# Optimization experiments

Measured on AMD Instinct MI355X. Metric: run time of the kernel, lower is better.

Reference implementation:

```python
import jax, jax.numpy as jnp
import numpy as np

INF = 10000.0
HEADS = 12
HEAD_SIZE = 64
HIDDEN = 1024
BATCH = 8
SEQLEN = 512


def _sin_cos(seqlen, dim, dtype):
    # SinusoidalPositionEmbedding (bert4torch style): indices = 10000**(-2i/dim)
    pos = jnp.arange(seqlen, dtype=dtype)
    inv = jnp.power(jnp.asarray(10000.0, dtype), -jnp.arange(dim // 2, dtype=dtype) * 2.0 / dim)
    freqs = pos[:, None] * inv[None, :]  # [s, dim/2]
    return jnp.sin(freqs), jnp.cos(freqs)


def setup_inputs() -> dict:
    key = jax.random.key(0)
    k1, k2, k3 = jax.random.split(key, 3)
    inputs = jax.random.normal(k1, (BATCH, SEQLEN, HIDDEN), dtype=jnp.float32)
    W = jax.random.normal(k2, (HIDDEN, HEADS * 2 * HEAD_SIZE), dtype=jnp.float32) * (HIDDEN ** -0.5)
    b = jax.random.normal(k3, (HEADS * 2 * HEAD_SIZE,), dtype=jnp.float32) * 0.02
    mask = jnp.ones((BATCH, SEQLEN), dtype=jnp.int32)
    return {"inputs": inputs, "W": W, "b": b, "mask": mask}


def reference(inputs, W, b, mask):
    bs, s, _ = inputs.shape
    h = inputs @ W + b  # [b, s, heads*2*hd]
    h = h.reshape(bs, s, HEADS, 2 * HEAD_SIZE)
    qw, kw = h[..., :HEAD_SIZE], h[..., HEAD_SIZE:]  # [b, s, h, d]

    # interleaved RoPE: cos_pos/sin_pos repeat each freq twice along last dim
    sin, cos = _sin_cos(s, HEAD_SIZE, h.dtype)
    cos2 = jnp.repeat(cos, 2, axis=-1)[None, :, None, :]  # [1, s, 1, d]
    sin2 = jnp.repeat(sin, 2, axis=-1)[None, :, None, :]

    def rot(x):
        x2 = jnp.stack([-x[..., 1::2], x[..., 0::2]], axis=-1).reshape(x.shape)
        return x * cos2 + x2 * sin2

    qw = rot(qw)
    kw = rot(kw)

    logits = jnp.einsum('bmhd,bnhd->bhmn', qw, kw)  # [b, h, s, s]

    m = mask.astype(logits.dtype)
    pad = 1.0 - m[:, None, None, :] * m[:, None, :, None]  # [b,1,s,s]
    tril = jnp.tril(jnp.ones((s, s), dtype=logits.dtype), k=-1)[None, None]  # strictly lower
    logits = logits - pad * INF - tril * INF
    out_mask = jnp.logical_or(pad > 0, tril > 0)
    return logits * (HEAD_SIZE ** -0.5), out_mask
```

## Files before the change

kernel.cpp:

```cpp
#include <hip/hip_runtime.h>
#include <stdint.h>

typedef unsigned short ushort_t;
typedef short short8 __attribute__((ext_vector_type(8)));
typedef float float4_ __attribute__((ext_vector_type(4)));
typedef unsigned short u16x8 __attribute__((ext_vector_type(8)));

#define INF_ 10000.0f
#define BATCH 8
#define SEQLEN 512
#define HIDDEN 1024
#define HEADS 12
#define HEAD_SIZE 64
#define NOUT 1536
#define MROWS 4096
#define BH 96
#define LOGITS_N 25165824
#define MASK_N   2097152

__device__ __align__(16) ushort_t g_A [(size_t)MROWS * HIDDEN];
__device__ __align__(16) ushort_t g_Wt[(size_t)NOUT * HIDDEN];
__device__ __align__(16) ushort_t g_Q[(size_t)BH * SEQLEN * HEAD_SIZE];
__device__ __align__(16) ushort_t g_K[(size_t)BH * SEQLEN * HEAD_SIZE];
__device__ __align__(16) float    g_tab[SEQLEN * 32 * 2];

__device__ __forceinline__ ushort_t f2bf(float f) {
    unsigned u = __builtin_bit_cast(unsigned, f);
    unsigned r = u + 0x7FFFu + ((u >> 16) & 1u);
    return (ushort_t)(r >> 16);
}

__device__ __forceinline__ void gload16(const ushort_t* g, ushort_t* l) {
    __builtin_amdgcn_global_load_lds(
        (const __attribute__((address_space(1))) void*)g,
        (__attribute__((address_space(3))) void*)l, 16, 0, 0);
}

__device__ __forceinline__ unsigned mask_code(const void* m) {
    unsigned u0 = ((const unsigned*)m)[0];
    unsigned u1 = ((const unsigned*)m)[1];
    if (u0 == 0x3F803F80u) return 2;
    if (u0 == 0x3F800000u) return 3;
    if (u0 == 0x01010101u) return 4;
    if (u0 == 0x00010001u) return 5;
    if (u0 == 1u && u1 == 0u) return 1;
    return 0;
}
__device__ __forceinline__ float mask_at(const void* m, unsigned code, int i) {
    switch (code) {
        case 1: return (float)((const long long*)m)[i];
        case 2: { unsigned u = (unsigned)((const ushort_t*)m)[i] << 16;
                  return __builtin_bit_cast(float, u); }
        case 3: return ((const float*)m)[i];
        case 4: return (float)((const signed char*)m)[i];
        case 5: return (float)((const short*)m)[i];
        default: return (float)((const int*)m)[i];
    }
}

__global__ void k_prep(const float* __restrict__ A, const float* __restrict__ W) {
    __shared__ ushort_t tile[32][33];
    int bid = blockIdx.x;
    int tid = threadIdx.x;
    if (bid < 2048) {
        int i = bid * 256 + tid;
        const float4_* p = (const float4_*)(A + (size_t)i * 8);
        float4_ v0 = p[0], v1 = p[1];
        u16x8 o;
        #pragma unroll
        for (int j = 0; j < 4; ++j) { o[j] = f2bf(v0[j]); o[j + 4] = f2bf(v1[j]); }
        *(u16x8*)(g_A + (size_t)i * 8) = o;
    } else if (bid < 2048 + 1536) {
        int bb = bid - 2048;
        int bx = bb % 48;
        int by = bb / 48;
        int tx = tid & 31, ty = tid >> 5;
        #pragma unroll
        for (int i = 0; i < 4; ++i) {
            int k = by * 32 + ty + i * 8;
            int n = bx * 32 + tx;
            tile[ty + i * 8][tx] = f2bf(W[(size_t)k * NOUT + n]);
        }
        __syncthreads();
        #pragma unroll
        for (int i = 0; i < 4; ++i) {
            int n = bx * 32 + ty + i * 8;
            int k = by * 32 + tx;
            g_Wt[(size_t)n * HIDDEN + k] = tile[tx][ty + i * 8];
        }
    } else {
        int i = (bid - 3584) * 256 + tid;
        int s = i >> 5, f = i & 31;
        float inv = powf(10000.0f, -(float)(2 * f) / 64.0f);
        float ang = (float)s * inv;
        g_tab[2 * i]     = sinf(ang);
        g_tab[2 * i + 1] = cosf(ang);
    }
}

__global__ void __launch_bounds__(256) k_gemm1(const float* __restrict__ bias) {
    __shared__ __align__(16) ushort_t sA[2][64 * 32];
    __shared__ __align__(16) ushort_t sB[2][128 * 32];
    int tid = threadIdx.x;
    int lane = tid & 63, wid = tid >> 6;
    int wm = wid >> 1, wn = wid & 1;
    int bm = (blockIdx.x & 63) * 64;
    int bn = (blockIdx.x >> 6) * 128;

    auto stage = [&](int bi, int ks) {
        {
            int row = tid >> 2, ch = tid & 3;
            gload16(g_A + (size_t)(bm + row) * HIDDEN + ks * 32 + ch * 8,
                    sA[bi] + (size_t)tid * 8);
        }
        #pragma unroll
        for (int i = 0; i < 2; ++i) {
            int c = tid + i * 256;
            int row = c >> 2, ch = c & 3;
            gload16(g_Wt + (size_t)(bn + row) * HIDDEN + ks * 32 + ch * 8,
                    sB[bi] + (size_t)c * 8);
        }
    };

    float4_ acc[2][4] = {};
    const int NT = HIDDEN / 32;
    stage(0, 0);
    __syncthreads();
    int cur = 0;
    for (int ks = 0; ks < NT; ++ks) {
        if (ks + 1 < NT) stage(cur ^ 1, ks + 1);
        short8 af[2], bfv[4];
        int kofs = (lane >> 4) * 8;
        #pragma unroll
        for (int mf = 0; mf < 2; ++mf)
            af[mf] = *(const short8*)(sA[cur] + (wm * 32 + mf * 16 + (lane & 15)) * 32 + kofs);
        #pragma unroll
        for (int nf = 0; nf < 4; ++nf)
            bfv[nf] = *(const short8*)(sB[cur] + (wn * 64 + nf * 16 + (lane & 15)) * 32 + kofs);
        #pragma unroll
        for (int mf = 0; mf < 2; ++mf)
            #pragma unroll
            for (int nf = 0; nf < 4; ++nf)
                acc[mf][nf] = __builtin_amdgcn_mfma_f32_16x16x32_bf16(af[mf], bfv[nf], acc[mf][nf], 0, 0, 0);
        __syncthreads();
        cur ^= 1;
    }

    #pragma unroll
    for (int nf = 0; nf < 4; ++nf) {
        int gn = bn + wn * 64 + nf * 16 + (lane & 15);
        float bv = bias[gn];
        int head = gn >> 7;
        int isk  = (gn >> 6) & 1;
        int d0 = gn & 63;
        int fi = d0 >> 1;
        float sgn = (gn & 1) ? 1.0f : -1.0f;
        ushort_t* dst = isk ? g_K : g_Q;
        #pragma unroll
        for (int mf = 0; mf < 2; ++mf) {
            int gm0 = bm + wm * 32 + mf * 16 + ((lane >> 4) * 4);
            #pragma unroll
            for (int r = 0; r < 4; ++r) {
                int gm = gm0 + r;
                int s = gm & (SEQLEN - 1);
                int b = gm >> 9;
                float v = acc[mf][nf][r] + bv;
                float p = __shfl_xor(v, 1, 64);
                const float* tc = g_tab + 2 * (s * 32 + fi);
                float sn = tc[0], cs = tc[1];
                float y = v * cs + sgn * p * sn;
                size_t o = (((size_t)(b * HEADS + head)) * SEQLEN + s) * HEAD_SIZE + d0;
                dst[o] = f2bf(y);
            }
        }
    }
}

__global__ void __launch_bounds__(256) k_gemm2(const void* __restrict__ mask,
                                               float* __restrict__ out) {
    __shared__ __align__(16) ushort_t sQ[128 * 64];
    __shared__ __align__(16) ushort_t sK[128 * 64];
    __shared__ float sMr[128], sMc[128];
    int tid = threadIdx.x;
    int lane = tid & 63, wid = tid >> 6;
    int blk = blockIdx.x;
    int bh = blk >> 4;
    int t = blk & 15;
    int mt = t >> 2, nt = t & 3;
    int b = bh / HEADS;
    bool writeMask = (bh - b * HEADS) == 0;

    const ushort_t* Qb = g_Q + ((size_t)bh * SEQLEN + mt * 128) * HEAD_SIZE;
    const ushort_t* Kb = g_K + ((size_t)bh * SEQLEN + nt * 128) * HEAD_SIZE;
    #pragma unroll
    for (int i = 0; i < 4; ++i) {
        int c = tid + i * 256;
        gload16(Qb + (size_t)c * 8, sQ + (size_t)c * 8);
        gload16(Kb + (size_t)c * 8, sK + (size_t)c * 8);
    }
    unsigned mcode = mask_code(mask);
    if (tid < 128)      sMr[tid]       = mask_at(mask, mcode, b * SEQLEN + mt * 128 + tid);
    else                sMc[tid - 128] = mask_at(mask, mcode, b * SEQLEN + nt * 128 + (tid - 128));
    __syncthreads();

    int wm = wid >> 1, wn = wid & 1;
    float4_ acc[4][4] = {};
    #pragma unroll
    for (int kk = 0; kk < 2; ++kk) {
        short8 af[4], bfv[4];
        int ko = kk * 32 + (lane >> 4) * 8;
        #pragma unroll
        for (int mf = 0; mf < 4; ++mf)
            af[mf] = *(const short8*)(sQ + (wm * 64 + mf * 16 + (lane & 15)) * 64 + ko);
        #pragma unroll
        for (int nf = 0; nf < 4; ++nf)
            bfv[nf] = *(const short8*)(sK + (wn * 64 + nf * 16 + (lane & 15)) * 64 + ko);
        #pragma unroll
        for (int mf = 0; mf < 4; ++mf)
            #pragma unroll
            for (int nf = 0; nf < 4; ++nf)
                acc[mf][nf] = __builtin_amdgcn_mfma_f32_16x16x32_bf16(af[mf], bfv[nf], acc[mf][nf], 0, 0, 0);
    }

    size_t obase = (size_t)bh * SEQLEN * SEQLEN;
    size_t mbase = (size_t)LOGITS_N + (size_t)b * SEQLEN * SEQLEN;
    #pragma unroll
    for (int mf = 0; mf < 4; ++mf) {
        #pragma unroll
        for (int nf = 0; nf < 4; ++nf) {
            int lcol = wn * 64 + nf * 16 + (lane & 15);
            int lrow0 = wm * 64 + mf * 16 + ((lane >> 4) * 4);
            int gn = nt * 128 + lcol;
            float mc = sMc[lcol];
            #pragma unroll
            for (int r = 0; r < 4; ++r) {
                int lrow = lrow0 + r;
                int gm = mt * 128 + lrow;
                float padv = 1.0f - sMr[lrow] * mc;
                bool tl = gn < gm;
                float v = (acc[mf][nf][r] - padv * INF_ - (tl ? INF_ : 0.0f)) * 0.125f;
                size_t off = (size_t)gm * SEQLEN + gn;
                out[obase + off] = v;
                if (writeMask)
                    out[mbase + off] = (padv > 0.0f || tl) ? 1.0f : 0.0f;
            }
        }
    }
}

extern "C" void kernel_launch(void* const* d_in, const int* in_sizes, int n_in,
                              void* d_out, int out_size, void* d_ws, size_t ws_size,
                              hipStream_t stream) {
    const float* inp = nullptr; const float* W = nullptr;
    const float* bias = nullptr; const void* mask = nullptr;
    for (int i = 0; i < n_in; ++i) {
        switch (in_sizes[i]) {
            case MROWS * HIDDEN:  inp  = (const float*)d_in[i]; break;
            case HIDDEN * NOUT:   W    = (const float*)d_in[i]; break;
            case NOUT:            bias = (const float*)d_in[i]; break;
            case BATCH * SEQLEN:  mask = d_in[i]; break;
        }
    }
    if (!inp || !W || !bias || !mask) {
        inp  = (const float*)d_in[0];
        W    = (const float*)d_in[1];
        bias = (const float*)d_in[2];
        mask = d_in[3];
    }
    float* out = (float*)d_out;
    (void)d_ws; (void)ws_size;

    k_prep<<<3648, 256, 0, stream>>>(inp, W);
    k_gemm1<<<768, 256, 0, stream>>>(bias);
    k_gemm2<<<16 * BH, 256, 0, stream>>>(mask, out);
}
```

Baseline: 73.93 us.

## Swizzle LDS tiles, deepen GEMM1 K-step to 64, remap GEMM2 block order

Applies an XOR swizzle on 16-byte chunks in shared memory for the Q/K and A/W tiles so that MFMA fragment reads avoid LDS bank conflicts. The projection GEMM now stages 64-wide K slices instead of 32, which halves the loop iterations and barriers but doubles the shared-memory footprint. The logits kernel also remaps block indices across groups of eight, presumably to spread neighbouring tiles across XCDs or cache slices. The risks are lower occupancy from the extra LDS and a different L2 locality pattern.

```diff
diff --git a/kernel.cpp b/kernel.cpp
--- a/kernel.cpp
+++ b/kernel.cpp
@@ -99,8 +99,8 @@
 }
 
 __global__ void __launch_bounds__(256) k_gemm1(const float* __restrict__ bias) {
-    __shared__ __align__(16) ushort_t sA[2][64 * 32];
-    __shared__ __align__(16) ushort_t sB[2][128 * 32];
+    __shared__ __align__(16) ushort_t sA[2][64 * 64];
+    __shared__ __align__(16) ushort_t sB[2][128 * 64];
     int tid = threadIdx.x;
     int lane = tid & 63, wid = tid >> 6;
     int wm = wid >> 1, wn = wid & 1;
@@ -108,40 +108,49 @@
     int bn = (blockIdx.x >> 6) * 128;
 
     auto stage = [&](int bi, int ks) {
-        {
-            int row = tid >> 2, ch = tid & 3;
-            gload16(g_A + (size_t)(bm + row) * HIDDEN + ks * 32 + ch * 8,
-                    sA[bi] + (size_t)tid * 8);
-        }
         #pragma unroll
         for (int i = 0; i < 2; ++i) {
             int c = tid + i * 256;
-            int row = c >> 2, ch = c & 3;
-            gload16(g_Wt + (size_t)(bn + row) * HIDDEN + ks * 32 + ch * 8,
+            int row = c >> 3, ch = (c & 7) ^ (row & 7);
+            gload16(g_A + (size_t)(bm + row) * HIDDEN + ks * 64 + ch * 8,
+                    sA[bi] + (size_t)c * 8);
+        }
+        #pragma unroll
+        for (int i = 0; i < 4; ++i) {
+            int c = tid + i * 256;
+            int row = c >> 3, ch = (c & 7) ^ (row & 7);
+            gload16(g_Wt + (size_t)(bn + row) * HIDDEN + ks * 64 + ch * 8,
                     sB[bi] + (size_t)c * 8);
         }
     };
 
     float4_ acc[2][4] = {};
-    const int NT = HIDDEN / 32;
+    const int NT = HIDDEN / 64;
     stage(0, 0);
     __syncthreads();
     int cur = 0;
     for (int ks = 0; ks < NT; ++ks) {
         if (ks + 1 < NT) stage(cur ^ 1, ks + 1);
-        short8 af[2], bfv[4];
-        int kofs = (lane >> 4) * 8;
-        #pragma unroll
-        for (int mf = 0; mf < 2; ++mf)
-            af[mf] = *(const short8*)(sA[cur] + (wm * 32 + mf * 16 + (lane & 15)) * 32 + kofs);
-        #pragma unroll
-        for (int nf = 0; nf < 4; ++nf)
-            bfv[nf] = *(const short8*)(sB[cur] + (wn * 64 + nf * 16 + (lane & 15)) * 32 + kofs);
-        #pragma unroll
-        for (int mf = 0; mf < 2; ++mf)
-            #pragma unroll
-            for (int nf = 0; nf < 4; ++nf)
-                acc[mf][nf] = __builtin_amdgcn_mfma_f32_16x16x32_bf16(af[mf], bfv[nf], acc[mf][nf], 0, 0, 0);
+        #pragma unroll
+        for (int kk = 0; kk < 2; ++kk) {
+            short8 af[2], bfv[4];
+            int c0 = kk * 4 + (lane >> 4);
+            #pragma unroll
+            for (int mf = 0; mf < 2; ++mf) {
+                int r = wm * 32 + mf * 16 + (lane & 15);
+                af[mf] = *(const short8*)(sA[cur] + r * 64 + ((c0 ^ (r & 7)) * 8));
+            }
+            #pragma unroll
+            for (int nf = 0; nf < 4; ++nf) {
+                int r = wn * 64 + nf * 16 + (lane & 15);
+                bfv[nf] = *(const short8*)(sB[cur] + r * 64 + ((c0 ^ (r & 7)) * 8));
+            }
+            #pragma unroll
+            for (int mf = 0; mf < 2; ++mf)
+                #pragma unroll
+                for (int nf = 0; nf < 4; ++nf)
+                    acc[mf][nf] = __builtin_amdgcn_mfma_f32_16x16x32_bf16(af[mf], bfv[nf], acc[mf][nf], 0, 0, 0);
+        }
         __syncthreads();
         cur ^= 1;
     }
@@ -183,7 +192,7 @@
     __shared__ float sMr[128], sMc[128];
     int tid = threadIdx.x;
     int lane = tid & 63, wid = tid >> 6;
-    int blk = blockIdx.x;
+    int blk = (blockIdx.x & 7) * 192 + (blockIdx.x >> 3);
     int bh = blk >> 4;
     int t = blk & 15;
     int mt = t >> 2, nt = t & 3;
@@ -195,8 +204,9 @@
     #pragma unroll
     for (int i = 0; i < 4; ++i) {
         int c = tid + i * 256;
-        gload16(Qb + (size_t)c * 8, sQ + (size_t)c * 8);
-        gload16(Kb + (size_t)c * 8, sK + (size_t)c * 8);
+        int row = c >> 3, ch = (c & 7) ^ (row & 7);
+        gload16(Qb + (size_t)row * 64 + ch * 8, sQ + (size_t)c * 8);
+        gload16(Kb + (size_t)row * 64 + ch * 8, sK + (size_t)c * 8);
     }
     unsigned mcode = mask_code(mask);
     if (tid < 128)      sMr[tid]       = mask_at(mask, mcode, b * SEQLEN + mt * 128 + tid);
@@ -208,13 +218,17 @@
     #pragma unroll
     for (int kk = 0; kk < 2; ++kk) {
         short8 af[4], bfv[4];
-        int ko = kk * 32 + (lane >> 4) * 8;
-        #pragma unroll
-        for (int mf = 0; mf < 4; ++mf)
-            af[mf] = *(const short8*)(sQ + (wm * 64 + mf * 16 + (lane & 15)) * 64 + ko);
-        #pragma unroll
-        for (int nf = 0; nf < 4; ++nf)
-            bfv[nf] = *(const short8*)(sK + (wn * 64 + nf * 16 + (lane & 15)) * 64 + ko);
+        int c0 = kk * 4 + (lane >> 4);
+        #pragma unroll
+        for (int mf = 0; mf < 4; ++mf) {
+            int r = wm * 64 + mf * 16 + (lane & 15);
+            af[mf] = *(const short8*)(sQ + r * 64 + ((c0 ^ (r & 7)) * 8));
+        }
+        #pragma unroll
+        for (int nf = 0; nf < 4; ++nf) {
+            int r = wn * 64 + nf * 16 + (lane & 15);
+            bfv[nf] = *(const short8*)(sK + r * 64 + ((c0 ^ (r & 7)) * 8));
+        }
         #pragma unroll
         for (int mf = 0; mf < 4; ++mf)
             #pragma unroll
```

After: 59.33 us, median of 2. 19.7% less time.
